# Kernel tuning notes

Measured on AMD Instinct MI355X. Metric: run time of the kernel, lower is better.

Reference implementation:

```python
import jax, jax.numpy as jnp
import numpy as np

B, S, D, H, M = 4, 1024, 1024, 16, 64
DH = D // H

def setup_inputs() -> dict:
    key = jax.random.key(0)
    ks = jax.random.split(key, 11)
    inp = {
        'q': jax.random.normal(ks[0], (B, S, D), jnp.float32),
        'k': jax.random.normal(ks[1], (B, S, D), jnp.float32),
        'v': jax.random.normal(ks[2], (B, S, D), jnp.float32),
        'q_mult': jax.random.normal(ks[3], (B, S, M), jnp.float32),
        'kv_mult': jax.random.normal(ks[4], (B, S, M), jnp.float32),
        'valid_lens': jax.random.randint(ks[5], (B,), 1, S, jnp.int32),
        'Wq': jax.random.normal(ks[6], (D, D), jnp.float32) / np.sqrt(D),
        'Wk': jax.random.normal(ks[7], (D, D), jnp.float32) / np.sqrt(D),
        'Wv': jax.random.normal(ks[8], (D, D), jnp.float32) / np.sqrt(D),
        'Wo': jax.random.normal(ks[9], (D, D), jnp.float32) / np.sqrt(D),
        'alpha_mult': jnp.ones((1,), jnp.float32),
    }
    return inp

def _split_heads(x):
    # [B,S,D] -> [B*H, S, DH]
    return x.reshape(B, S, H, DH).transpose(0, 2, 1, 3).reshape(B * H, S, DH)

def reference(q, k, v, q_mult, kv_mult, valid_lens, Wq, Wk, Wv, Wo, alpha_mult):
    qh = _split_heads(q @ Wq)
    kh = _split_heads(k @ Wk)
    vh = _split_heads(v @ Wv)

    # outer-product bias term with Frobenius normalization
    kvm = kv_mult * alpha_mult
    mult = jnp.einsum('bqm,bkm->bqk', q_mult, kvm)  # [B,S,S]
    fro = jnp.sqrt(jnp.sum(mult * mult, axis=(1, 2), keepdims=True))
    mult = mult / (fro + 1e-5)
    mult = jnp.repeat(mult, H, axis=0)  # [B*H,S,S]

    scores = jnp.einsum('bqd,bkd->bqk', qh, kh) / jnp.sqrt(jnp.float32(DH))

    # masked softmax over key axis (set masked to -1e6, matching torch impl)
    vl = jnp.repeat(valid_lens, H)  # [B*H]
    mask = jnp.arange(S)[None, None, :] < vl[:, None, None]
    scores = jnp.where(mask, scores, jnp.float32(-1e6))
    attn = jax.nn.softmax(scores, axis=-1) + mult  # after_softmax=True path

    out = jnp.einsum('bqk,bkd->bqd', attn, vh)  # [B*H,S,DH]
    out = out.reshape(B, H, S, DH).transpose(0, 2, 1, 3).reshape(B, S, D)
    return out @ Wo
```

## Files before the change

### kernel.cpp

```cpp
#include <hip/hip_runtime.h>
#include <hip/hip_bf16.h>
#include <stdint.h>

#define SB 1024
#define DD 1024
#define NH 16
#define MM 64
#define DHD 64

typedef __attribute__((ext_vector_type(8))) short s16x8;
typedef __attribute__((ext_vector_type(4))) float f32x4;

__device__ __forceinline__ unsigned short f2bf(float f) {
    union { float f; unsigned int u; } v; v.f = f;
    unsigned int u = v.u;
    u += 0x7FFFu + ((u >> 16) & 1u);
    return (unsigned short)(u >> 16);
}

__device__ __forceinline__ void gload_lds16(const unsigned short* g, unsigned short* l) {
    __builtin_amdgcn_global_load_lds(
        (const __attribute__((address_space(1))) unsigned int*)g,
        (__attribute__((address_space(3))) unsigned int*)l, 16, 0, 0);
}

__global__ __launch_bounds__(256) void cvtw_kernel(const float* q, const float* k, const float* v,
                                                   unsigned short* qb, unsigned short* kb,
                                                   unsigned short* vb,
                                                   const float* W0, const float* W1,
                                                   const float* W2, const float* W3,
                                                   unsigned short* Wt) {
    const int bid = blockIdx.x, tid = threadIdx.x;
    __shared__ float tile[32][33];
    if (bid < 6144) {
        const int z = bid >> 11;
        const float* src = (z == 0) ? q : (z == 1) ? k : v;
        unsigned short* dst = (z == 0) ? qb : (z == 1) ? kb : vb;
        const size_t base = ((size_t)(bid & 2047) * 256 + tid) * 8;
        f32x4 a = *(const f32x4*)(src + base);
        f32x4 b2 = *(const f32x4*)(src + base + 4);
        s16x8 t;
        t[0] = (short)f2bf(a[0]);  t[1] = (short)f2bf(a[1]);
        t[2] = (short)f2bf(a[2]);  t[3] = (short)f2bf(a[3]);
        t[4] = (short)f2bf(b2[0]); t[5] = (short)f2bf(b2[1]);
        t[6] = (short)f2bf(b2[2]); t[7] = (short)f2bf(b2[3]);
        *(s16x8*)(dst + base) = t;
    } else {
        const int wt = bid - 6144;
        const int z = wt >> 10, rem = wt & 1023;
        const int x0 = (rem & 31) * 32, y0 = (rem >> 5) * 32;
        const float* W = (z == 0) ? W0 : (z == 1) ? W1 : (z == 2) ? W2 : W3;
        unsigned short* Wo_ = Wt + (size_t)z * DD * DD;
        const int tx = tid & 31, ty = tid >> 5;
#pragma unroll
        for (int j = 0; j < 4; ++j)
            tile[ty + 8 * j][tx] = W[(size_t)(y0 + ty + 8 * j) * DD + x0 + tx];
        __syncthreads();
#pragma unroll
        for (int j = 0; j < 4; ++j)
            Wo_[(size_t)(x0 + ty + 8 * j) * DD + y0 + tx] = f2bf(tile[tx][ty + 8 * j]);
    }
}

typedef unsigned short LdsTile[2][2][128][64];

template <int OMODE>
__device__ __forceinline__ void gemm_body(const unsigned short* A, const unsigned short* Bt,
                                          void* outp, int m0b, int n0b, LdsTile& lds) {
    const int tid = threadIdx.x, l = tid & 63, w = tid >> 6;
    const int l15 = l & 15, lq = l >> 4;
    const int wm = (w >> 1) * 32, wn = (w & 1) * 64;
    const int ric = l >> 3;
    const int gsrc = (l & 7) ^ (ric & 7);

    f32x4 acc[2][4];
#pragma unroll
    for (int i = 0; i < 2; ++i)
#pragma unroll
        for (int j = 0; j < 4; ++j) acc[i][j] = (f32x4){0.f, 0.f, 0.f, 0.f};

    auto STAGE = [&](int bb, int kt) {
        const int k0 = kt * 64;
#pragma unroll
        for (int j = 0; j < 2; ++j) {
            const int chunk = w * 2 + j;
            const int r = chunk * 8 + ric;
            gload_lds16(A + (size_t)(m0b + r) * DD + k0 + gsrc * 8, &lds[bb][0][chunk * 8][0]);
            gload_lds16(Bt + (size_t)(n0b + r) * DD + k0 + gsrc * 8, &lds[bb][1][chunk * 8][0]);
        }
    };

    STAGE(0, 0);
    __syncthreads();
    int cur = 0;
    for (int kt = 0; kt < 16; ++kt) {
        if (kt < 15) STAGE(cur ^ 1, kt + 1);
#pragma unroll
        for (int kt2 = 0; kt2 < 2; ++kt2) {
            s16x8 af[2], bf[4];
#pragma unroll
            for (int mi = 0; mi < 2; ++mi) {
                const int R = wm + mi * 16 + l15;
                af[mi] = *(const s16x8*)(&lds[cur][0][R][((kt2 * 4 + lq) ^ (R & 7)) * 8]);
            }
#pragma unroll
            for (int ni = 0; ni < 4; ++ni) {
                const int R = wn + ni * 16 + l15;
                bf[ni] = *(const s16x8*)(&lds[cur][1][R][((kt2 * 4 + lq) ^ (R & 7)) * 8]);
            }
#pragma unroll
            for (int mi = 0; mi < 2; ++mi)
#pragma unroll
                for (int ni = 0; ni < 4; ++ni)
                    acc[mi][ni] = __builtin_amdgcn_mfma_f32_16x16x32_bf16(af[mi], bf[ni],
                                                                          acc[mi][ni], 0, 0, 0);
        }
        __syncthreads();
        cur ^= 1;
    }

#pragma unroll
    for (int mi = 0; mi < 2; ++mi)
#pragma unroll
        for (int ni = 0; ni < 4; ++ni)
#pragma unroll
            for (int i = 0; i < 4; ++i) {
                const int r = m0b + wm + mi * 16 + lq * 4 + i;
                const int c = n0b + wn + ni * 16 + l15;
                const float vv = acc[mi][ni][i];
                if (OMODE == 2) {
                    ((float*)outp)[(size_t)r * DD + c] = vv;
                } else {
                    const int b = r >> 10, s = r & 1023;
                    const int hh = c >> 6, dh = c & 63;
                    if (OMODE == 0)
                        ((unsigned short*)outp)[((size_t)((b * NH + hh) * SB + s)) * DHD + dh] = f2bf(vv);
                    else
                        ((unsigned short*)outp)[((size_t)((b * NH + hh) * DHD + dh)) * SB + s] = f2bf(vv);
                }
            }
}

__device__ __forceinline__ void xcd_decode(int i, int& m0b, int& n0b) {
    const int xcd = i & 7, idx = i >> 3;
    m0b = (xcd * 4 + (idx >> 3)) * 128;
    n0b = (idx & 7) * 128;
}

__global__ __launch_bounds__(512, 4) void gemm_qkv_kernel(const unsigned short* qb,
                                                          const unsigned short* kb,
                                                          const unsigned short* vb,
                                                          const unsigned short* Wt,
                                                          unsigned short* qhp, unsigned short* khp,
                                                          unsigned short* vht) {
    __shared__ LdsTile lds;
    const int wg = blockIdx.x;
    const int t = wg >> 8, i = wg & 255;
    int m0b, n0b;
    xcd_decode(i, m0b, n0b);
    const unsigned short* Bt = Wt + (size_t)t * DD * DD;
    if (t == 0)      gemm_body<0>(qb, Bt, qhp, m0b, n0b, lds);
    else if (t == 1) gemm_body<0>(kb, Bt, khp, m0b, n0b, lds);
    else             gemm_body<1>(vb, Bt, vht, m0b, n0b, lds);
}

__global__ __launch_bounds__(512, 4) void gemm_o_kernel(const unsigned short* aout,
                                                        const unsigned short* WtO, float* out) {
    __shared__ LdsTile lds;
    int m0b, n0b;
    xcd_decode(blockIdx.x, m0b, n0b);
    gemm_body<2>(aout, WtO, out, m0b, n0b, lds);
}

__global__ __launch_bounds__(256) void ukgram_kernel(const unsigned short* vht, const float* qm,
                                                     const float* kvm, const float* alpha_p,
                                                     unsigned short* U, float* cscale) {
    __shared__ char lds_raw[81952];
    float (*part)[64][64] = (float (*)[64][64])lds_raw;
    float (*gq)[64] = (float (*)[64])(lds_raw + 65536);
    float* red = (float*)(lds_raw + 81920);

    const int bid = blockIdx.x;
    const int tid = threadIdx.x, l = tid & 63, w = tid >> 6;
    const int l15 = l & 15, lq = l >> 4;

    if (bid < 64) {
        const int bh = bid, b = bh >> 4;
        f32x4 acc[4][4];
#pragma unroll
        for (int i = 0; i < 4; ++i)
#pragma unroll
            for (int j = 0; j < 4; ++j) acc[i][j] = (f32x4){0.f, 0.f, 0.f, 0.f};
        for (int kt2 = 0; kt2 < 8; ++kt2) {
            const int sbase = w * 256 + kt2 * 32 + 8 * lq;
            s16x8 av[4], bk[4];
#pragma unroll
            for (int t = 0; t < 4; ++t)
                av[t] = *(const s16x8*)(vht + ((size_t)bh * DHD + t * 16 + l15) * SB + sbase);
#pragma unroll
            for (int t = 0; t < 4; ++t) {
                s16x8 tmp;
#pragma unroll
                for (int j = 0; j < 8; ++j)
                    tmp[j] = (short)f2bf(kvm[((size_t)b * SB + sbase + j) * MM + t * 16 + l15]);
                bk[t] = tmp;
            }
#pragma unroll
            for (int at = 0; at < 4; ++at)
#pragma unroll
                for (int bt = 0; bt < 4; ++bt)
                    acc[at][bt] = __builtin_amdgcn_mfma_f32_16x16x32_bf16(av[at], bk[bt],
                                                                          acc[at][bt], 0, 0, 0);
        }
#pragma unroll
        for (int at = 0; at < 4; ++at)
#pragma unroll
            for (int bt = 0; bt < 4; ++bt)
#pragma unroll
                for (int i = 0; i < 4; ++i)
                    part[w][at * 16 + lq * 4 + i][bt * 16 + l15] = acc[at][bt][i];
        __syncthreads();
        for (int e = tid * 16; e < tid * 16 + 16; ++e) {
            const int r = e >> 6, c = e & 63;
            U[(size_t)bh * 4096 + e] =
                f2bf(part[0][r][c] + part[1][r][c] + part[2][r][c] + part[3][r][c]);
        }
    } else {
        const int b = bid - 64;
        f32x4 acc[4][4];
#pragma unroll
        for (int i = 0; i < 4; ++i)
#pragma unroll
            for (int j = 0; j < 4; ++j) acc[i][j] = (f32x4){0.f, 0.f, 0.f, 0.f};
        for (int kt2 = 0; kt2 < 8; ++kt2) {
            const int sbase = w * 256 + kt2 * 32 + 8 * lq;
            s16x8 fq[4];
#pragma unroll
            for (int t = 0; t < 4; ++t) {
                s16x8 tmp;
#pragma unroll
                for (int j = 0; j < 8; ++j)
                    tmp[j] = (short)f2bf(qm[((size_t)b * SB + sbase + j) * MM + t * 16 + l15]);
                fq[t] = tmp;
            }
#pragma unroll
            for (int at = 0; at < 4; ++at)
#pragma unroll
                for (int bt = 0; bt < 4; ++bt)
                    acc[at][bt] = __builtin_amdgcn_mfma_f32_16x16x32_bf16(fq[at], fq[bt],
                                                                         acc[at][bt], 0, 0, 0);
        }
#pragma unroll
        for (int at = 0; at < 4; ++at)
#pragma unroll
            for (int bt = 0; bt < 4; ++bt)
#pragma unroll
                for (int i = 0; i < 4; ++i)
                    part[w][at * 16 + lq * 4 + i][bt * 16 + l15] = acc[at][bt][i];
        __syncthreads();
        for (int e = tid * 16; e < tid * 16 + 16; ++e) {
            const int r = e >> 6, c = e & 63;
            gq[r][c] = part[0][r][c] + part[1][r][c] + part[2][r][c] + part[3][r][c];
        }
        __syncthreads();
#pragma unroll
        for (int i = 0; i < 4; ++i)
#pragma unroll
            for (int j = 0; j < 4; ++j) acc[i][j] = (f32x4){0.f, 0.f, 0.f, 0.f};
        for (int kt2 = 0; kt2 < 8; ++kt2) {
            const int sbase = w * 256 + kt2 * 32 + 8 * lq;
            s16x8 fk[4];
#pragma unroll
            for (int t = 0; t < 4; ++t) {
                s16x8 tmp;
#pragma unroll
                for (int j = 0; j < 8; ++j)
                    tmp[j] = (short)f2bf(kvm[((size_t)b * SB + sbase + j) * MM + t * 16 + l15]);
                fk[t] = tmp;
            }
#pragma unroll
            for (int at = 0; at < 4; ++at)
#pragma unroll
                for (int bt = 0; bt < 4; ++bt)
                    acc[at][bt] = __builtin_amdgcn_mfma_f32_16x16x32_bf16(fk[at], fk[bt],
                                                                         acc[at][bt], 0, 0, 0);
        }
#pragma unroll
        for (int at = 0; at < 4; ++at)
#pragma unroll
            for (int bt = 0; bt < 4; ++bt)
#pragma unroll
                for (int i = 0; i < 4; ++i)
                    part[w][at * 16 + lq * 4 + i][bt * 16 + l15] = acc[at][bt][i];
        __syncthreads();
        float ss = 0.f;
        for (int e = tid * 16; e < tid * 16 + 16; ++e) {
            const int r = e >> 6, c = e & 63;
            const float gk = part[0][r][c] + part[1][r][c] + part[2][r][c] + part[3][r][c];
            ss += gk * gq[r][c];
        }
#pragma unroll
        for (int mk = 1; mk < 64; mk <<= 1) ss += __shfl_xor(ss, mk);
        if (l == 0) red[w] = ss;
        __syncthreads();
        if (tid == 0) {
            const float S = red[0] + red[1] + red[2] + red[3];
            const float a = alpha_p[0];
            cscale[b] = a / (sqrtf(a * a * S) + 1e-5f);
        }
    }
}

__global__ __launch_bounds__(512, 6) void attn_kernel(const unsigned short* qh, const unsigned short* kh,
                                                      const unsigned short* vht, const unsigned short* U,
                                                      const float* cscale, const float* qm,
                                                      const int* valid_lens, unsigned short* aout) {
    const int wg = blockIdx.x;
    const int xcd = wg & 7, ii = wg >> 3;
    const int bh = (ii >> 3) * 8 + xcd;
    const int q0 = (ii & 7) * 128;
    const int b = bh >> 4, h = bh & 15;
    const int tid = threadIdx.x, l = tid & 63, w = tid >> 6;
    const int l15 = l & 15, lq = l >> 4;
    const int vl = valid_lens[b];
    const float cs = cscale[b];
    const int ntile = (vl + 63) >> 6;

    __shared__ unsigned short Kt[2][64][64];
    __shared__ unsigned short Vt[2][64][64];
    __shared__ unsigned short Pl[8][16][64];

    const int sr = tid >> 3;
    const int gs = (tid & 7) ^ (sr & 7);
    const unsigned short* khb = kh + (size_t)bh * SB * DHD;
    const unsigned short* vhb = vht + (size_t)bh * DHD * SB;

    auto STAGE = [&](int bb, int t) {
        const int kv0 = t << 6;
        gload_lds16(khb + (size_t)(kv0 + sr) * DHD + gs * 8, &Kt[bb][w * 8][0]);
        gload_lds16(vhb + (size_t)sr * SB + kv0 + gs * 8, &Vt[bb][w * 8][0]);
    };

    s16x8 aq[2];
#pragma unroll
    for (int kt = 0; kt < 2; ++kt)
        aq[kt] = *(const s16x8*)(qh + ((size_t)bh * SB + q0 + w * 16 + l15) * DHD + kt * 32 + 8 * lq);

    float l_[4];
    f32x4 oacc[4];
#pragma unroll
    for (int i = 0; i < 4; ++i) l_[i] = 0.f;
#pragma unroll
    for (int nd = 0; nd < 4; ++nd) oacc[nd] = (f32x4){0.f, 0.f, 0.f, 0.f};

    STAGE(0, 0);
    __syncthreads();
    int cur = 0;
    for (int t = 0; t < ntile; ++t) {
        if (t + 1 < ntile) STAGE(cur ^ 1, t + 1);
        const int kv0 = t << 6;
        const bool bdry = (kv0 + 64 > vl);

        f32x4 sc[4];
#pragma unroll
        for (int nt = 0; nt < 4; ++nt) {
            const int r = nt * 16 + l15;
            s16x8 b0 = *(const s16x8*)(&Kt[cur][r][((lq) ^ (r & 7)) * 8]);
            s16x8 b1 = *(const s16x8*)(&Kt[cur][r][((4 + lq) ^ (r & 7)) * 8]);
            f32x4 z = (f32x4){0.f, 0.f, 0.f, 0.f};
            z = __builtin_amdgcn_mfma_f32_16x16x32_bf16(aq[0], b0, z, 0, 0, 0);
            sc[nt] = __builtin_amdgcn_mfma_f32_16x16x32_bf16(aq[1], b1, z, 0, 0, 0);
        }

#pragma unroll
        for (int nt = 0; nt < 4; ++nt) {
            const bool ok = !bdry || (kv0 + nt * 16 + l15 < vl);
#pragma unroll
            for (int i = 0; i < 4; ++i) {
                const float p = ok ? __expf(fmaf(sc[nt][i], 0.125f, -16.0f)) : 0.f;
                l_[i] += p;
                const int pr = lq * 4 + i;
                Pl[w][pr][(nt * 16 + l15) ^ (8 * (pr & 7))] = f2bf(p);
            }
        }

#pragma unroll
        for (int kt = 0; kt < 2; ++kt) {
            s16x8 pa = *(const s16x8*)(&Pl[w][l15][((kt * 4 + lq) ^ (l15 & 7)) * 8]);
#pragma unroll
            for (int nd = 0; nd < 4; ++nd) {
                const int r = nd * 16 + l15;
                s16x8 vb = *(const s16x8*)(&Vt[cur][r][((kt * 4 + lq) ^ (r & 7)) * 8]);
                oacc[nd] = __builtin_amdgcn_mfma_f32_16x16x32_bf16(pa, vb, oacc[nd], 0, 0, 0);
            }
        }
        __syncthreads();
        cur ^= 1;
    }

#pragma unroll
    for (int mk = 1; mk < 16; mk <<= 1)
#pragma unroll
        for (int i = 0; i < 4; ++i) l_[i] += __shfl_xor(l_[i], mk);

    s16x8 xa[2];
#pragma unroll
    for (int kt2 = 0; kt2 < 2; ++kt2) {
        const float* qp = qm + ((size_t)b * SB + q0 + w * 16 + l15) * MM + kt2 * 32 + 8 * lq;
        f32x4 qa = *(const f32x4*)qp;
        f32x4 qb2 = *(const f32x4*)(qp + 4);
        s16x8 at;
        at[0] = (short)f2bf(qa[0]);  at[1] = (short)f2bf(qa[1]);
        at[2] = (short)f2bf(qa[2]);  at[3] = (short)f2bf(qa[3]);
        at[4] = (short)f2bf(qb2[0]); at[5] = (short)f2bf(qb2[1]);
        at[6] = (short)f2bf(qb2[2]); at[7] = (short)f2bf(qb2[3]);
        xa[kt2] = at;
    }
    float rinv[4];
#pragma unroll
    for (int i = 0; i < 4; ++i) rinv[i] = 1.f / l_[i];
#pragma unroll
    for (int nd = 0; nd < 4; ++nd) {
        f32x4 xacc = (f32x4){0.f, 0.f, 0.f, 0.f};
#pragma unroll
        for (int kt2 = 0; kt2 < 2; ++kt2) {
            s16x8 bu = *(const s16x8*)(U + ((size_t)bh * 64 + nd * 16 + l15) * 64 + kt2 * 32 + 8 * lq);
            xacc = __builtin_amdgcn_mfma_f32_16x16x32_bf16(xa[kt2], bu, xacc, 0, 0, 0);
        }
#pragma unroll
        for (int i = 0; i < 4; ++i) {
            const int row = q0 + w * 16 + lq * 4 + i;
            const float val = oacc[nd][i] * rinv[i] + xacc[i] * cs;
            aout[((size_t)b * SB + row) * DD + h * DHD + nd * 16 + l15] = f2bf(val);
        }
    }
}

extern "C" void kernel_launch(void* const* d_in, const int* in_sizes, int n_in,
                              void* d_out, int out_size, void* d_ws, size_t ws_size,
                              hipStream_t stream) {
    const float* q   = (const float*)d_in[0];
    const float* k   = (const float*)d_in[1];
    const float* v   = (const float*)d_in[2];
    const float* qm  = (const float*)d_in[3];
    const float* kvm = (const float*)d_in[4];
    const int* vl    = (const int*)d_in[5];
    const float* Wq  = (const float*)d_in[6];
    const float* Wk  = (const float*)d_in[7];
    const float* Wv  = (const float*)d_in[8];
    const float* Wo  = (const float*)d_in[9];
    const float* alpha = (const float*)d_in[10];

    char* ws = (char*)d_ws;
    unsigned short* Wt  = (unsigned short*)(ws);
    unsigned short* qb  = (unsigned short*)(ws + ((size_t)8  << 20));
    unsigned short* kb  = (unsigned short*)(ws + ((size_t)16 << 20));
    unsigned short* vb  = (unsigned short*)(ws + ((size_t)24 << 20));
    unsigned short* qhp = (unsigned short*)(ws + ((size_t)32 << 20));
    unsigned short* khp = (unsigned short*)(ws + ((size_t)40 << 20));
    unsigned short* vht = (unsigned short*)(ws + ((size_t)48 << 20));
    unsigned short* U   = (unsigned short*)(ws + ((size_t)8  << 20));
    float* csc          = (float*)(ws + ((size_t)9 << 20));
    unsigned short* aout = (unsigned short*)(ws + ((size_t)16 << 20));

    cvtw_kernel<<<10240, 256, 0, stream>>>(q, k, v, qb, kb, vb, Wq, Wk, Wv, Wo, Wt);
    gemm_qkv_kernel<<<768, 512, 0, stream>>>(qb, kb, vb, Wt, qhp, khp, vht);
    ukgram_kernel<<<68, 256, 0, stream>>>(vht, qm, kvm, alpha, U, csc);
    attn_kernel<<<512, 512, 0, stream>>>(qhp, khp, vht, U, csc, qm, vl, aout);
    gemm_o_kernel<<<256, 512, 0, stream>>>(aout, Wt + 3 * (1u << 20), (float*)d_out);
}
```

Baseline: 215.1 us.

## Fold ukgram kernel into QKV GEMM launch via kvm^T·v precompute

Removes the separate ukgram launch. The U = Vh^T·kvm products are now computed as Wv_h^T·(v^T·kvm), with v^T·kvm precomputed in extra blocks of the conversion kernel. The U and Frobenius-norm blocks are appended to the QKV GEMM grid, so they no longer depend on vht and can run alongside the projection. The attention block-to-(bh,q0) mapping is also permuted to change L2/XCD locality. The cost is an extra GEMM stage of rounding error in U from the reassociation, and some tail imbalance in the enlarged launch.

```diff
diff --git a/kernel.cpp b/kernel.cpp
--- a/kernel.cpp
+++ b/kernel.cpp
@@ -29,7 +29,8 @@
                                                    unsigned short* vb,
                                                    const float* W0, const float* W1,
                                                    const float* W2, const float* W3,
-                                                   unsigned short* Wt) {
+                                                   unsigned short* Wt, const float* kvm,
+                                                   unsigned short* Tt) {
     const int bid = blockIdx.x, tid = threadIdx.x;
     __shared__ float tile[32][33];
     if (bid < 6144) {
@@ -45,7 +46,7 @@
         t[4] = (short)f2bf(b2[0]); t[5] = (short)f2bf(b2[1]);
         t[6] = (short)f2bf(b2[2]); t[7] = (short)f2bf(b2[3]);
         *(s16x8*)(dst + base) = t;
-    } else {
+    } else if (bid < 10240) {
         const int wt = bid - 6144;
         const int z = wt >> 10, rem = wt & 1023;
         const int x0 = (rem & 31) * 32, y0 = (rem >> 5) * 32;
@@ -59,6 +60,49 @@
 #pragma unroll
         for (int j = 0; j < 4; ++j)
             Wo_[(size_t)(x0 + ty + 8 * j) * DD + y0 + tx] = f2bf(tile[tx][ty + 8 * j]);
+    } else {
+        const int tb = bid - 10240;
+        const int b = tb >> 3, d0 = (tb & 7) * 128;
+        const int l = tid & 63, w = tid >> 6;
+        const int l15 = l & 15, lq = l >> 4;
+        f32x4 acc[4][2];
+#pragma unroll
+        for (int i = 0; i < 4; ++i)
+#pragma unroll
+            for (int j = 0; j < 2; ++j) acc[i][j] = (f32x4){0.f, 0.f, 0.f, 0.f};
+        for (int kt = 0; kt < 32; ++kt) {
+            const int sb_ = kt * 32 + 8 * lq;
+            s16x8 af[4];
+#pragma unroll
+            for (int at = 0; at < 4; ++at) {
+                s16x8 tmp;
+#pragma unroll
+                for (int j = 0; j < 8; ++j)
+                    tmp[j] = (short)f2bf(kvm[((size_t)(b * SB + sb_ + j)) * MM + at * 16 + l15]);
+                af[at] = tmp;
+            }
+#pragma unroll
+            for (int bt = 0; bt < 2; ++bt) {
+                s16x8 bv;
+#pragma unroll
+                for (int j = 0; j < 8; ++j)
+                    bv[j] = (short)f2bf(v[((size_t)(b * SB + sb_ + j)) * DD + d0 + (w * 2 + bt) * 16 + l15]);
+#pragma unroll
+                for (int at = 0; at < 4; ++at)
+                    acc[at][bt] = __builtin_amdgcn_mfma_f32_16x16x32_bf16(af[at], bv,
+                                                                          acc[at][bt], 0, 0, 0);
+            }
+        }
+#pragma unroll
+        for (int at = 0; at < 4; ++at)
+#pragma unroll
+            for (int bt = 0; bt < 2; ++bt)
+#pragma unroll
+                for (int i = 0; i < 4; ++i) {
+                    const int m = at * 16 + lq * 4 + i;
+                    const int d = d0 + (w * 2 + bt) * 16 + l15;
+                    Tt[((size_t)b * 64 + m) * DD + d] = f2bf(acc[at][bt][i]);
+                }
     }
 }
 
@@ -152,16 +196,161 @@
                                                           const unsigned short* vb,
                                                           const unsigned short* Wt,
                                                           unsigned short* qhp, unsigned short* khp,
-                                                          unsigned short* vht) {
+                                                          unsigned short* vht,
+                                                          const unsigned short* Tt, const float* qm,
+                                                          const float* kvm, const float* alpha_p,
+                                                          unsigned short* U, float* csc) {
     __shared__ LdsTile lds;
+    __shared__ float red2[8];
     const int wg = blockIdx.x;
-    const int t = wg >> 8, i = wg & 255;
-    int m0b, n0b;
-    xcd_decode(i, m0b, n0b);
-    const unsigned short* Bt = Wt + (size_t)t * DD * DD;
-    if (t == 0)      gemm_body<0>(qb, Bt, qhp, m0b, n0b, lds);
-    else if (t == 1) gemm_body<0>(kb, Bt, khp, m0b, n0b, lds);
-    else             gemm_body<1>(vb, Bt, vht, m0b, n0b, lds);
+    const int tid = threadIdx.x, l = tid & 63, w = tid >> 6;
+    const int l15 = l & 15, lq = l >> 4;
+
+    if (wg < 768) {
+        const int t = wg >> 8, i = wg & 255;
+        int m0b, n0b;
+        xcd_decode(i, m0b, n0b);
+        const unsigned short* Bt = Wt + (size_t)t * DD * DD;
+        if (t == 0)      gemm_body<0>(qb, Bt, qhp, m0b, n0b, lds);
+        else if (t == 1) gemm_body<0>(kb, Bt, khp, m0b, n0b, lds);
+        else             gemm_body<1>(vb, Bt, vht, m0b, n0b, lds);
+    } else if (wg < 832) {
+        const int bh = wg - 768, b = bh >> 4, h = bh & 15;
+        float (*part)[64][64] = (float (*)[64][64])(&lds[0][0][0][0]);
+        if (w < 4) {
+            const unsigned short* Wvt = Wt + (size_t)2 * DD * DD;
+            f32x4 acc[4][4];
+#pragma unroll
+            for (int i = 0; i < 4; ++i)
+#pragma unroll
+                for (int j = 0; j < 4; ++j) acc[i][j] = (f32x4){0.f, 0.f, 0.f, 0.f};
+            for (int kt2 = 0; kt2 < 8; ++kt2) {
+                const int kbase = w * 256 + kt2 * 32 + 8 * lq;
+                s16x8 af[4], bf[4];
+#pragma unroll
+                for (int at = 0; at < 4; ++at)
+                    af[at] = *(const s16x8*)(Wvt + (size_t)(h * 64 + at * 16 + l15) * DD + kbase);
+#pragma unroll
+                for (int bt = 0; bt < 4; ++bt)
+                    bf[bt] = *(const s16x8*)(Tt + ((size_t)b * 64 + bt * 16 + l15) * DD + kbase);
+#pragma unroll
+                for (int at = 0; at < 4; ++at)
+#pragma unroll
+                    for (int bt = 0; bt < 4; ++bt)
+                        acc[at][bt] = __builtin_amdgcn_mfma_f32_16x16x32_bf16(af[at], bf[bt],
+                                                                              acc[at][bt], 0, 0, 0);
+            }
+#pragma unroll
+            for (int at = 0; at < 4; ++at)
+#pragma unroll
+                for (int bt = 0; bt < 4; ++bt)
+#pragma unroll
+                    for (int i = 0; i < 4; ++i)
+                        part[w][at * 16 + lq * 4 + i][bt * 16 + l15] = acc[at][bt][i];
+        }
+        __syncthreads();
+#pragma unroll
+        for (int j = 0; j < 8; ++j) {
+            const int e = tid * 8 + j;
+            const int r = e >> 6, c = e & 63;
+            U[(size_t)bh * 4096 + e] =
+                f2bf(part[0][r][c] + part[1][r][c] + part[2][r][c] + part[3][r][c]);
+        }
+    } else {
+        const int b = wg - 832;
+        float (*part)[64][64] = (float (*)[64][64])(&lds[0][0][0][0]);
+        float gqr[8];
+        if (w < 4) {
+            f32x4 acc[4][4];
+#pragma unroll
+            for (int i = 0; i < 4; ++i)
+#pragma unroll
+                for (int j = 0; j < 4; ++j) acc[i][j] = (f32x4){0.f, 0.f, 0.f, 0.f};
+            for (int kt2 = 0; kt2 < 8; ++kt2) {
+                const int sbase = w * 256 + kt2 * 32 + 8 * lq;
+                s16x8 fq[4];
+#pragma unroll
+                for (int t = 0; t < 4; ++t) {
+                    s16x8 tmp;
+#pragma unroll
+                    for (int j = 0; j < 8; ++j)
+                        tmp[j] = (short)f2bf(qm[((size_t)b * SB + sbase + j) * MM + t * 16 + l15]);
+                    fq[t] = tmp;
+                }
+#pragma unroll
+                for (int at = 0; at < 4; ++at)
+#pragma unroll
+                    for (int bt = 0; bt < 4; ++bt)
+                        acc[at][bt] = __builtin_amdgcn_mfma_f32_16x16x32_bf16(fq[at], fq[bt],
+                                                                             acc[at][bt], 0, 0, 0);
+            }
+#pragma unroll
+            for (int at = 0; at < 4; ++at)
+#pragma unroll
+                for (int bt = 0; bt < 4; ++bt)
+#pragma unroll
+                    for (int i = 0; i < 4; ++i)
+                        part[w][at * 16 + lq * 4 + i][bt * 16 + l15] = acc[at][bt][i];
+        }
+        __syncthreads();
+#pragma unroll
+        for (int j = 0; j < 8; ++j) {
+            const int e = tid * 8 + j;
+            const int r = e >> 6, c = e & 63;
+            gqr[j] = part[0][r][c] + part[1][r][c] + part[2][r][c] + part[3][r][c];
+        }
+        __syncthreads();
+        if (w < 4) {
+            f32x4 acc[4][4];
+#pragma unroll
+            for (int i = 0; i < 4; ++i)
+#pragma unroll
+                for (int j = 0; j < 4; ++j) acc[i][j] = (f32x4){0.f, 0.f, 0.f, 0.f};
+            for (int kt2 = 0; kt2 < 8; ++kt2) {
+                const int sbase = w * 256 + kt2 * 32 + 8 * lq;
+                s16x8 fk[4];
+#pragma unroll
+                for (int t = 0; t < 4; ++t) {
+                    s16x8 tmp;
+#pragma unroll
+                    for (int j = 0; j < 8; ++j)
+                        tmp[j] = (short)f2bf(kvm[((size_t)b * SB + sbase + j) * MM + t * 16 + l15]);
+                    fk[t] = tmp;
+                }
+#pragma unroll
+                for (int at = 0; at < 4; ++at)
+#pragma unroll
+                    for (int bt = 0; bt < 4; ++bt)
+                        acc[at][bt] = __builtin_amdgcn_mfma_f32_16x16x32_bf16(fk[at], fk[bt],
+                                                                             acc[at][bt], 0, 0, 0);
+            }
+#pragma unroll
+            for (int at = 0; at < 4; ++at)
+#pragma unroll
+                for (int bt = 0; bt < 4; ++bt)
+#pragma unroll
+                    for (int i = 0; i < 4; ++i)
+                        part[w][at * 16 + lq * 4 + i][bt * 16 + l15] = acc[at][bt][i];
+        }
+        __syncthreads();
+        float ss = 0.f;
+#pragma unroll
+        for (int j = 0; j < 8; ++j) {
+            const int e = tid * 8 + j;
+            const int r = e >> 6, c = e & 63;
+            ss += (part[0][r][c] + part[1][r][c] + part[2][r][c] + part[3][r][c]) * gqr[j];
+        }
+#pragma unroll
+        for (int mk = 1; mk < 64; mk <<= 1) ss += __shfl_xor(ss, mk);
+        if (l == 0) red2[w] = ss;
+        __syncthreads();
+        if (tid == 0) {
+            const float S = red2[0] + red2[1] + red2[2] + red2[3] +
+                            red2[4] + red2[5] + red2[6] + red2[7];
+            const float a = alpha_p[0];
+            csc[b] = a / (sqrtf(a * a * S) + 1e-5f);
+        }
+    }
 }
 
 __global__ __launch_bounds__(512, 4) void gemm_o_kernel(const unsigned short* aout,
@@ -172,153 +361,15 @@
     gemm_body<2>(aout, WtO, out, m0b, n0b, lds);
 }
 
-__global__ __launch_bounds__(256) void ukgram_kernel(const unsigned short* vht, const float* qm,
-                                                     const float* kvm, const float* alpha_p,
-                                                     unsigned short* U, float* cscale) {
-    __shared__ char lds_raw[81952];
-    float (*part)[64][64] = (float (*)[64][64])lds_raw;
-    float (*gq)[64] = (float (*)[64])(lds_raw + 65536);
-    float* red = (float*)(lds_raw + 81920);
-
-    const int bid = blockIdx.x;
-    const int tid = threadIdx.x, l = tid & 63, w = tid >> 6;
-    const int l15 = l & 15, lq = l >> 4;
-
-    if (bid < 64) {
-        const int bh = bid, b = bh >> 4;
-        f32x4 acc[4][4];
-#pragma unroll
-        for (int i = 0; i < 4; ++i)
-#pragma unroll
-            for (int j = 0; j < 4; ++j) acc[i][j] = (f32x4){0.f, 0.f, 0.f, 0.f};
-        for (int kt2 = 0; kt2 < 8; ++kt2) {
-            const int sbase = w * 256 + kt2 * 32 + 8 * lq;
-            s16x8 av[4], bk[4];
-#pragma unroll
-            for (int t = 0; t < 4; ++t)
-                av[t] = *(const s16x8*)(vht + ((size_t)bh * DHD + t * 16 + l15) * SB + sbase);
-#pragma unroll
-            for (int t = 0; t < 4; ++t) {
-                s16x8 tmp;
-#pragma unroll
-                for (int j = 0; j < 8; ++j)
-                    tmp[j] = (short)f2bf(kvm[((size_t)b * SB + sbase + j) * MM + t * 16 + l15]);
-                bk[t] = tmp;
-            }
-#pragma unroll
-            for (int at = 0; at < 4; ++at)
-#pragma unroll
-                for (int bt = 0; bt < 4; ++bt)
-                    acc[at][bt] = __builtin_amdgcn_mfma_f32_16x16x32_bf16(av[at], bk[bt],
-                                                                          acc[at][bt], 0, 0, 0);
-        }
-#pragma unroll
-        for (int at = 0; at < 4; ++at)
-#pragma unroll
-            for (int bt = 0; bt < 4; ++bt)
-#pragma unroll
-                for (int i = 0; i < 4; ++i)
-                    part[w][at * 16 + lq * 4 + i][bt * 16 + l15] = acc[at][bt][i];
-        __syncthreads();
-        for (int e = tid * 16; e < tid * 16 + 16; ++e) {
-            const int r = e >> 6, c = e & 63;
-            U[(size_t)bh * 4096 + e] =
-                f2bf(part[0][r][c] + part[1][r][c] + part[2][r][c] + part[3][r][c]);
-        }
-    } else {
-        const int b = bid - 64;
-        f32x4 acc[4][4];
-#pragma unroll
-        for (int i = 0; i < 4; ++i)
-#pragma unroll
-            for (int j = 0; j < 4; ++j) acc[i][j] = (f32x4){0.f, 0.f, 0.f, 0.f};
-        for (int kt2 = 0; kt2 < 8; ++kt2) {
-            const int sbase = w * 256 + kt2 * 32 + 8 * lq;
-            s16x8 fq[4];
-#pragma unroll
-            for (int t = 0; t < 4; ++t) {
-                s16x8 tmp;
-#pragma unroll
-                for (int j = 0; j < 8; ++j)
-                    tmp[j] = (short)f2bf(qm[((size_t)b * SB + sbase + j) * MM + t * 16 + l15]);
-                fq[t] = tmp;
-            }
-#pragma unroll
-            for (int at = 0; at < 4; ++at)
-#pragma unroll
-                for (int bt = 0; bt < 4; ++bt)
-                    acc[at][bt] = __builtin_amdgcn_mfma_f32_16x16x32_bf16(fq[at], fq[bt],
-                                                                         acc[at][bt], 0, 0, 0);
-        }
-#pragma unroll
-        for (int at = 0; at < 4; ++at)
-#pragma unroll
-            for (int bt = 0; bt < 4; ++bt)
-#pragma unroll
-                for (int i = 0; i < 4; ++i)
-                    part[w][at * 16 + lq * 4 + i][bt * 16 + l15] = acc[at][bt][i];
-        __syncthreads();
-        for (int e = tid * 16; e < tid * 16 + 16; ++e) {
-            const int r = e >> 6, c = e & 63;
-            gq[r][c] = part[0][r][c] + part[1][r][c] + part[2][r][c] + part[3][r][c];
-        }
-        __syncthreads();
-#pragma unroll
-        for (int i = 0; i < 4; ++i)
-#pragma unroll
-            for (int j = 0; j < 4; ++j) acc[i][j] = (f32x4){0.f, 0.f, 0.f, 0.f};
-        for (int kt2 = 0; kt2 < 8; ++kt2) {
-            const int sbase = w * 256 + kt2 * 32 + 8 * lq;
-            s16x8 fk[4];
-#pragma unroll
-            for (int t = 0; t < 4; ++t) {
-                s16x8 tmp;
-#pragma unroll
-                for (int j = 0; j < 8; ++j)
-                    tmp[j] = (short)f2bf(kvm[((size_t)b * SB + sbase + j) * MM + t * 16 + l15]);
-                fk[t] = tmp;
-            }
-#pragma unroll
-            for (int at = 0; at < 4; ++at)
-#pragma unroll
-                for (int bt = 0; bt < 4; ++bt)
-                    acc[at][bt] = __builtin_amdgcn_mfma_f32_16x16x32_bf16(fk[at], fk[bt],
-                                                                         acc[at][bt], 0, 0, 0);
-        }
-#pragma unroll
-        for (int at = 0; at < 4; ++at)
-#pragma unroll
-            for (int bt = 0; bt < 4; ++bt)
-#pragma unroll
-                for (int i = 0; i < 4; ++i)
-                    part[w][at * 16 + lq * 4 + i][bt * 16 + l15] = acc[at][bt][i];
-        __syncthreads();
-        float ss = 0.f;
-        for (int e = tid * 16; e < tid * 16 + 16; ++e) {
-            const int r = e >> 6, c = e & 63;
-            const float gk = part[0][r][c] + part[1][r][c] + part[2][r][c] + part[3][r][c];
-            ss += gk * gq[r][c];
-        }
-#pragma unroll
-        for (int mk = 1; mk < 64; mk <<= 1) ss += __shfl_xor(ss, mk);
-        if (l == 0) red[w] = ss;
-        __syncthreads();
-        if (tid == 0) {
-            const float S = red[0] + red[1] + red[2] + red[3];
-            const float a = alpha_p[0];
-            cscale[b] = a / (sqrtf(a * a * S) + 1e-5f);
-        }
-    }
-}
-
 __global__ __launch_bounds__(512, 6) void attn_kernel(const unsigned short* qh, const unsigned short* kh,
                                                       const unsigned short* vht, const unsigned short* U,
                                                       const float* cscale, const float* qm,
                                                       const int* valid_lens, unsigned short* aout) {
     const int wg = blockIdx.x;
     const int xcd = wg & 7, ii = wg >> 3;
-    const int bh = (ii >> 3) * 8 + xcd;
-    const int q0 = (ii & 7) * 128;
+    const int r3 = ((ii & 1) << 2) | (ii & 2) | ((ii & 4) >> 2);
+    const int bh = r3 * 8 + xcd;
+    const int q0 = (ii >> 3) * 128;
     const int b = bh >> 4, h = bh & 15;
     const int tid = threadIdx.x, l = tid & 63, w = tid >> 6;
     const int l15 = l & 15, lq = l >> 4;
@@ -459,13 +510,14 @@
     unsigned short* qhp = (unsigned short*)(ws + ((size_t)32 << 20));
     unsigned short* khp = (unsigned short*)(ws + ((size_t)40 << 20));
     unsigned short* vht = (unsigned short*)(ws + ((size_t)48 << 20));
-    unsigned short* U   = (unsigned short*)(ws + ((size_t)8  << 20));
-    float* csc          = (float*)(ws + ((size_t)9 << 20));
+    unsigned short* U   = (unsigned short*)(ws + ((size_t)56 << 20));
+    unsigned short* Tt  = (unsigned short*)(ws + ((size_t)57 << 20));
+    float* csc          = (float*)(ws + ((size_t)58 << 20));
     unsigned short* aout = (unsigned short*)(ws + ((size_t)16 << 20));
 
-    cvtw_kernel<<<10240, 256, 0, stream>>>(q, k, v, qb, kb, vb, Wq, Wk, Wv, Wo, Wt);
-    gemm_qkv_kernel<<<768, 512, 0, stream>>>(qb, kb, vb, Wt, qhp, khp, vht);
-    ukgram_kernel<<<68, 256, 0, stream>>>(vht, qm, kvm, alpha, U, csc);
+    cvtw_kernel<<<10272, 256, 0, stream>>>(q, k, v, qb, kb, vb, Wq, Wk, Wv, Wo, Wt, kvm, Tt);
+    gemm_qkv_kernel<<<836, 512, 0, stream>>>(qb, kb, vb, Wt, qhp, khp, vht,
+                                             Tt, qm, kvm, alpha, U, csc);
     attn_kernel<<<512, 512, 0, stream>>>(qhp, khp, vht, U, csc, qm, vl, aout);
     gemm_o_kernel<<<256, 512, 0, stream>>>(aout, Wt + 3 * (1u << 20), (float*)d_out);
 }
```

New measurement: 252.4 us. 1.17x slower.
